# Performance work log

Hardware: AMD Instinct MI355X
Metric: run time of the kernel (lower is better)

The kernel has to match this reference:

```python
import jax, jax.numpy as jnp
import numpy as np

N_NODES = 50000
BN_EPS = 1e-5


def setup_inputs() -> dict:
    key = jax.random.key(0)
    ks = jax.random.split(key, 10)
    n, e, d, L = N_NODES, 500000, 128, 2
    x = jax.random.normal(ks[0], (n, d), dtype=jnp.float32)
    edge_index = jax.random.randint(ks[1], (2, e), 0, n, dtype=jnp.int64)
    edge_attr = jax.random.normal(ks[2], (e, d), dtype=jnp.float32)
    W1 = jax.random.normal(ks[3], (L, d, d), dtype=jnp.float32) * 0.05
    b1 = jax.random.normal(ks[4], (L, d), dtype=jnp.float32) * 0.02
    gamma = 1.0 + 0.1 * jax.random.normal(ks[5], (L, d), dtype=jnp.float32)
    beta = 0.1 * jax.random.normal(ks[6], (L, d), dtype=jnp.float32)
    W2 = jax.random.normal(ks[7], (L, d, d), dtype=jnp.float32) * 0.05
    b2 = jax.random.normal(ks[8], (L, d), dtype=jnp.float32) * 0.02
    return {"x": x, "edge_index": edge_index, "edge_attr": edge_attr,
            "W1": W1, "b1": b1, "gamma": gamma, "beta": beta, "W2": W2, "b2": b2}


def _gine_layer(x, src, dst, edge_attr, W1l, b1l, gl, bl, W2l, b2l):
    # GINEConv message: relu(x_j + edge_attr), sum-aggregated to target nodes
    msg = jax.nn.relu(x[src] + edge_attr)              # [E, d]
    agg = jax.ops.segment_sum(msg, dst, num_segments=N_NODES)  # [N, d]
    h = (x + agg) @ W1l + b1l                           # eps=0 -> (1+eps)*x = x
    # BatchNorm1d over nodes (train-mode batch stats, biased var)
    mu = jnp.mean(h, axis=0)
    var = jnp.mean(jnp.square(h - mu), axis=0)
    h = (h - mu) * jax.lax.rsqrt(var + BN_EPS) * gl + bl
    h = jax.nn.relu(h)
    h = jax.nn.relu(h @ W2l + b2l)
    return jax.nn.relu(h)  # encoder's outer activation


def reference(x, edge_index, edge_attr, W1, b1, gamma, beta, W2, b2):
    src, dst = edge_index[0], edge_index[1]
    L = W1.shape[0]
    for l in range(L):
        x = _gine_layer(x, src, dst, edge_attr, W1[l], b1[l], gamma[l], beta[l], W2[l], b2[l])
    return x
```

## Files before the change

kernel.cpp:

```cpp
#include <hip/hip_runtime.h>

#define BN_EPS 1e-5f

using f4 = __attribute__((ext_vector_type(4))) float;

__device__ inline f4 relu4(f4 v) {
    v.x = fmaxf(v.x, 0.f); v.y = fmaxf(v.y, 0.f);
    v.z = fmaxf(v.z, 0.f); v.w = fmaxf(v.w, 0.f);
    return v;
}

__global__ __launch_bounds__(256) void detect_i64_kernel(const int* __restrict__ ei,
                                                         int* __restrict__ flag, int npairs) {
    __shared__ int ok;
    if (threadIdx.x == 0) ok = 1;
    __syncthreads();
    bool bad = false;
    for (int i = threadIdx.x; i < npairs; i += 256)
        bad |= (ei[2 * i + 1] != 0);
    if (bad) ok = 0;
    __syncthreads();
    if (threadIdx.x == 0) *flag = ok;
}

__global__ __launch_bounds__(256) void canon_kernel(const int* __restrict__ ei,
                                                    const int* __restrict__ flag,
                                                    int* __restrict__ canon,
                                                    int* __restrict__ deg, int n2, int N) {
    int i = blockIdx.x * 256 + threadIdx.x;
    if (i < N) deg[i] = 0;
    if (i >= n2) return;
    int wide = *flag;
    canon[i] = wide ? ei[2 * i] : ei[i];
}

__global__ __launch_bounds__(256) void hist_kernel(const int* __restrict__ dst,
                                                   int* __restrict__ deg, int E) {
    int e = blockIdx.x * 256 + threadIdx.x;
    if (e >= E) return;
    atomicAdd(&deg[dst[e]], 1);
}

__global__ __launch_bounds__(1024) void scan_kernel(const int* __restrict__ deg,
                                                    int* __restrict__ rowptr,
                                                    int* __restrict__ cursor, int N) {
    __shared__ int part[1024];
    int t = threadIdx.x;
    int chunk = (N + 1023) / 1024;
    int lo = t * chunk;
    int hi = lo + chunk;
    if (lo > N) lo = N;
    if (hi > N) hi = N;
    int s = 0;
    for (int i = lo; i < hi; ++i) s += deg[i];
    part[t] = s;
    __syncthreads();
    for (int off = 1; off < 1024; off <<= 1) {
        int v = (t >= off) ? part[t - off] : 0;
        __syncthreads();
        part[t] += v;
        __syncthreads();
    }
    int run = (t == 0) ? 0 : part[t - 1];
    for (int i = lo; i < hi; ++i) { rowptr[i] = run; cursor[i] = run; run += deg[i]; }
    if (t == 1023) rowptr[N] = run;
}

__global__ __launch_bounds__(256) void fill_kernel(const int* __restrict__ src,
                                                   const int* __restrict__ dst,
                                                   int* __restrict__ cursor,
                                                   int2* __restrict__ pbuf, int E) {
    int e = blockIdx.x * 256 + threadIdx.x;
    if (e >= E) return;
    int d = dst[e];
    int pos = atomicAdd(&cursor[d], 1);
    pbuf[pos] = make_int2(e, src[e]);
}

__global__ __launch_bounds__(256) void gather_kernel(const float* __restrict__ x,
                                                     const float* __restrict__ ea,
                                                     const int* __restrict__ rowptr,
                                                     const int2* __restrict__ pbuf,
                                                     float* __restrict__ aggx,
                                                     float* __restrict__ sums, int N) {
    if (blockIdx.x == 0) sums[threadIdx.x] = 0.f;
    int t = blockIdx.x * 256 + threadIdx.x;
    int n = t >> 5;
    if (n >= N) return;
    int f = t & 31;
    int lo = rowptr[n], hi = rowptr[n + 1];
    f4 acc0 = ((const f4*)(x + (size_t)n * 128))[f];
    f4 acc1 = {0.f, 0.f, 0.f, 0.f};
    int i = lo;
    for (; i + 2 <= hi; i += 2) {
        int2 p0 = pbuf[i];
        int2 p1 = pbuf[i + 1];
        f4 xv0 = ((const f4*)(x + (size_t)p0.y * 128))[f];
        f4 av0 = __builtin_nontemporal_load(((const f4*)(ea + (size_t)p0.x * 128)) + f);
        f4 xv1 = ((const f4*)(x + (size_t)p1.y * 128))[f];
        f4 av1 = __builtin_nontemporal_load(((const f4*)(ea + (size_t)p1.x * 128)) + f);
        acc0 += relu4(xv0 + av0);
        acc1 += relu4(xv1 + av1);
    }
    if (i < hi) {
        int2 p0 = pbuf[i];
        f4 xv0 = ((const f4*)(x + (size_t)p0.y * 128))[f];
        f4 av0 = __builtin_nontemporal_load(((const f4*)(ea + (size_t)p0.x * 128)) + f);
        acc0 += relu4(xv0 + av0);
    }
    f4 r = acc0 + acc1;
    ((f4*)(aggx + (size_t)n * 128))[f] = r;
}

template <int MODE>
__global__ __launch_bounds__(256) void gemm_kernel(const float* __restrict__ A,
                                                   const float* __restrict__ W,
                                                   const float* __restrict__ bias,
                                                   float* __restrict__ sums,
                                                   const float* __restrict__ gamma,
                                                   const float* __restrict__ beta,
                                                   float* __restrict__ out, int N,
                                                   float invN) {
    __shared__ float sA[64][132];
    __shared__ float sW[32][128];
    __shared__ float sScale[128];
    __shared__ float sShift[128];
    int t = threadIdx.x;
    int rbase = blockIdx.x * 64;

    if (MODE == 2) {
        if (t < 128) {
            float mean = sums[t] * invN;
            float var = sums[128 + t] * invN - mean * mean;
            float inv = rsqrtf(var + BN_EPS);
            float sc = gamma[t] * inv;
            sScale[t] = sc;
            sShift[t] = beta[t] - mean * sc;
        }
        __syncthreads();
    }

    {
        int colq = t & 31;
        int r0 = t >> 5;
        float4 s4 = make_float4(0.f, 0.f, 0.f, 0.f), sh4 = make_float4(0.f, 0.f, 0.f, 0.f);
        if (MODE == 2) {
            s4 = reinterpret_cast<const float4*>(sScale)[colq];
            sh4 = reinterpret_cast<const float4*>(sShift)[colq];
        }
#pragma unroll
        for (int it = 0; it < 8; ++it) {
            int r = r0 + it * 8;
            int row = rbase + r;
            float4 v = make_float4(0.f, 0.f, 0.f, 0.f);
            if (row < N) {
                float4 a = reinterpret_cast<const float4*>(A + (size_t)row * 128)[colq];
                if (MODE == 1) {
                    v = a;
                } else {
                    v.x = fmaxf(a.x * s4.x + sh4.x, 0.f);
                    v.y = fmaxf(a.y * s4.y + sh4.y, 0.f);
                    v.z = fmaxf(a.z * s4.z + sh4.z, 0.f);
                    v.w = fmaxf(a.w * s4.w + sh4.w, 0.f);
                }
            }
            *reinterpret_cast<float4*>(&sA[r][colq * 4]) = v;
        }
    }

    float acc[4][8];
#pragma unroll
    for (int r = 0; r < 4; ++r)
#pragma unroll
        for (int c = 0; c < 8; ++c) acc[r][c] = 0.f;

    int cg = t & 15, rg = t >> 4;
    int c0a = cg * 4;
    int c0b = 64 + cg * 4;

    for (int kc = 0; kc < 4; ++kc) {
        __syncthreads();
#pragma unroll
        for (int pass = 0; pass < 4; ++pass) {
            int kk = (t >> 5) + pass * 8;
            int k = kc * 32 + kk;
            float4 w = reinterpret_cast<const float4*>(W + (size_t)k * 128)[t & 31];
            *reinterpret_cast<float4*>(&sW[kk][(t & 31) * 4]) = w;
        }
        __syncthreads();
#pragma unroll
        for (int kk0 = 0; kk0 < 32; kk0 += 4) {
            float4 a[4];
#pragma unroll
            for (int r = 0; r < 4; ++r)
                a[r] = *reinterpret_cast<const float4*>(&sA[rg * 4 + r][kc * 32 + kk0]);
#pragma unroll
            for (int j = 0; j < 4; ++j) {
                float4 w0 = *reinterpret_cast<const float4*>(&sW[kk0 + j][c0a]);
                float4 w1 = *reinterpret_cast<const float4*>(&sW[kk0 + j][c0b]);
#pragma unroll
                for (int r = 0; r < 4; ++r) {
                    float av = (j == 0) ? a[r].x : (j == 1) ? a[r].y : (j == 2) ? a[r].z : a[r].w;
                    acc[r][0] += av * w0.x;
                    acc[r][1] += av * w0.y;
                    acc[r][2] += av * w0.z;
                    acc[r][3] += av * w0.w;
                    acc[r][4] += av * w1.x;
                    acc[r][5] += av * w1.y;
                    acc[r][6] += av * w1.z;
                    acc[r][7] += av * w1.w;
                }
            }
        }
    }

    float4 b0 = *reinterpret_cast<const float4*>(bias + c0a);
    float4 b1v = *reinterpret_cast<const float4*>(bias + c0b);
    float cs[8], cs2[8];
#pragma unroll
    for (int j = 0; j < 8; ++j) { cs[j] = 0.f; cs2[j] = 0.f; }

#pragma unroll
    for (int r = 0; r < 4; ++r) {
        int row = rbase + rg * 4 + r;
        if (row >= N) continue;
        float4 o0, o1;
        o0.x = acc[r][0] + b0.x;  o0.y = acc[r][1] + b0.y;
        o0.z = acc[r][2] + b0.z;  o0.w = acc[r][3] + b0.w;
        o1.x = acc[r][4] + b1v.x; o1.y = acc[r][5] + b1v.y;
        o1.z = acc[r][6] + b1v.z; o1.w = acc[r][7] + b1v.w;
        if (MODE == 2) {
            o0.x = fmaxf(o0.x, 0.f); o0.y = fmaxf(o0.y, 0.f);
            o0.z = fmaxf(o0.z, 0.f); o0.w = fmaxf(o0.w, 0.f);
            o1.x = fmaxf(o1.x, 0.f); o1.y = fmaxf(o1.y, 0.f);
            o1.z = fmaxf(o1.z, 0.f); o1.w = fmaxf(o1.w, 0.f);
        } else {
            cs[0] += o0.x; cs2[0] += o0.x * o0.x;
            cs[1] += o0.y; cs2[1] += o0.y * o0.y;
            cs[2] += o0.z; cs2[2] += o0.z * o0.z;
            cs[3] += o0.w; cs2[3] += o0.w * o0.w;
            cs[4] += o1.x; cs2[4] += o1.x * o1.x;
            cs[5] += o1.y; cs2[5] += o1.y * o1.y;
            cs[6] += o1.z; cs2[6] += o1.z * o1.z;
            cs[7] += o1.w; cs2[7] += o1.w * o1.w;
        }
        *reinterpret_cast<float4*>(out + (size_t)row * 128 + c0a) = o0;
        *reinterpret_cast<float4*>(out + (size_t)row * 128 + c0b) = o1;
    }

    if (MODE == 1) {
        __syncthreads();
        float* red = &sA[0][0];
        float* red2 = red + 2048;
        int base = (rg * 16 + cg) * 8;
#pragma unroll
        for (int j = 0; j < 8; ++j) { red[base + j] = cs[j]; red2[base + j] = cs2[j]; }
        __syncthreads();
        if (t < 128) {
            int cgj = (t & 63) >> 2;
            int j = (t & 3) + ((t >> 6) << 2);
            float s = 0.f, s2 = 0.f;
#pragma unroll
            for (int rr = 0; rr < 16; ++rr) {
                s += red[(rr * 16 + cgj) * 8 + j];
                s2 += red2[(rr * 16 + cgj) * 8 + j];
            }
            unsafeAtomicAdd(&sums[t], s);
            unsafeAtomicAdd(&sums[128 + t], s2);
        }
    }
}

extern "C" void kernel_launch(void* const* d_in, const int* in_sizes, int n_in,
                              void* d_out, int out_size, void* d_ws, size_t ws_size,
                              hipStream_t stream) {
    const float* x     = (const float*)d_in[0];
    const int*   ei    = (const int*)d_in[1];
    const float* ea    = (const float*)d_in[2];
    const float* W1    = (const float*)d_in[3];
    const float* b1    = (const float*)d_in[4];
    const float* gamma = (const float*)d_in[5];
    const float* beta  = (const float*)d_in[6];
    const float* W2    = (const float*)d_in[7];
    const float* b2    = (const float*)d_in[8];

    int N = in_sizes[0] / 128;
    int E = in_sizes[2] / 128;
    int L = in_sizes[3] / (128 * 128);

    size_t NF = (size_t)N * 128;
    float* aggx  = (float*)d_ws;
    float* h     = aggx + NF;
    float* sums  = h + NF;
    int*   canon  = (int*)(sums + 256);
    int*   deg    = canon + (size_t)2 * E;
    int*   rowptr = deg + N;
    int*   cursor = rowptr + N + 2;
    int2*  pbuf   = (int2*)(cursor + N);
    int*   flag   = (int*)(pbuf + E);

    int npairs = (E < 4096) ? E : 4096;
    detect_i64_kernel<<<1, 256, 0, stream>>>(ei, flag, npairs);
    int E2 = 2 * E;
    int m = (E2 > N) ? E2 : N;
    canon_kernel<<<(m + 255) / 256, 256, 0, stream>>>(ei, flag, canon, deg, E2, N);
    const int* src = canon;
    const int* dst = canon + E;

    int eBlocks = (E + 255) / 256;
    hist_kernel<<<eBlocks, 256, 0, stream>>>(dst, deg, E);
    scan_kernel<<<1, 1024, 0, stream>>>(deg, rowptr, cursor, N);
    fill_kernel<<<eBlocks, 256, 0, stream>>>(src, dst, cursor, pbuf, E);

    int gatherBlocks = (N * 32 + 255) / 256;
    int gemmBlocks = (N + 63) / 64;
    float invN = 1.0f / (float)N;
    const float* xin = x;
    for (int l = 0; l < L; ++l) {
        float* xout = (float*)d_out;
        gather_kernel<<<gatherBlocks, 256, 0, stream>>>(xin, ea, rowptr, pbuf, aggx, sums, N);
        gemm_kernel<1><<<gemmBlocks, 256, 0, stream>>>(aggx, W1 + (size_t)l * 16384,
                                                       b1 + (size_t)l * 128, sums,
                                                       nullptr, nullptr, h, N, invN);
        gemm_kernel<2><<<gemmBlocks, 256, 0, stream>>>(h, W2 + (size_t)l * 16384,
                                                       b2 + (size_t)l * 128, sums,
                                                       gamma + (size_t)l * 128,
                                                       beta + (size_t)l * 128, xout, N, invN);
        xin = xout;
    }
}
```

Before: 777.7 us.

## Fuse degree histogram into canon, parallelize CSR scan, unroll gather by four

Moves zeroing of the degree array into the detect kernel and folds the destination histogram atomics into the canonicalization kernel, which removes one launch and one pass over dst. The single-block 1024-thread serial-chunk scan is replaced by a three-kernel multi-block scan (block scan, partials scan, add-back). The gather loop is unrolled to four edges with four accumulators to increase memory-level parallelism. This adds two small launches, and the single-block detect kernel now zeroes all N degrees serially over 256 threads.

```diff
diff --git a/kernel.cpp b/kernel.cpp
--- a/kernel.cpp
+++ b/kernel.cpp
@@ -11,7 +11,8 @@
 }
 
 __global__ __launch_bounds__(256) void detect_i64_kernel(const int* __restrict__ ei,
-                                                         int* __restrict__ flag, int npairs) {
+                                                         int* __restrict__ flag, int npairs,
+                                                         int* __restrict__ deg, int N) {
     __shared__ int ok;
     if (threadIdx.x == 0) ok = 1;
     __syncthreads();
@@ -19,6 +20,10 @@
     for (int i = threadIdx.x; i < npairs; i += 256)
         bad |= (ei[2 * i + 1] != 0);
     if (bad) ok = 0;
+    int nq = N >> 2;
+    int4* d4 = (int4*)deg;
+    for (int i = threadIdx.x; i < nq; i += 256) d4[i] = make_int4(0, 0, 0, 0);
+    for (int i = (nq << 2) + threadIdx.x; i < N; i += 256) deg[i] = 0;
     __syncthreads();
     if (threadIdx.x == 0) *flag = ok;
 }
@@ -26,44 +31,83 @@
 __global__ __launch_bounds__(256) void canon_kernel(const int* __restrict__ ei,
                                                     const int* __restrict__ flag,
                                                     int* __restrict__ canon,
-                                                    int* __restrict__ deg, int n2, int N) {
+                                                    int* __restrict__ deg, int n2, int E) {
     int i = blockIdx.x * 256 + threadIdx.x;
-    if (i < N) deg[i] = 0;
     if (i >= n2) return;
     int wide = *flag;
-    canon[i] = wide ? ei[2 * i] : ei[i];
-}
-
-__global__ __launch_bounds__(256) void hist_kernel(const int* __restrict__ dst,
-                                                   int* __restrict__ deg, int E) {
-    int e = blockIdx.x * 256 + threadIdx.x;
-    if (e >= E) return;
-    atomicAdd(&deg[dst[e]], 1);
-}
-
-__global__ __launch_bounds__(1024) void scan_kernel(const int* __restrict__ deg,
-                                                    int* __restrict__ rowptr,
-                                                    int* __restrict__ cursor, int N) {
-    __shared__ int part[1024];
+    int v = wide ? ei[2 * i] : ei[i];
+    canon[i] = v;
+    if (i >= E) atomicAdd(&deg[v], 1);
+}
+
+__global__ __launch_bounds__(256) void scan_blk_kernel(const int* __restrict__ deg,
+                                                       int* __restrict__ rowptr,
+                                                       int* __restrict__ partials, int N) {
+    __shared__ int s[256];
+    int b = blockIdx.x, t = threadIdx.x;
+    int base = b * 1024 + t * 4;
+    int4 v = make_int4(0, 0, 0, 0);
+    if (base + 3 < N) v = *(const int4*)(deg + base);
+    else {
+        if (base < N) v.x = deg[base];
+        if (base + 1 < N) v.y = deg[base + 1];
+        if (base + 2 < N) v.z = deg[base + 2];
+        if (base + 3 < N) v.w = deg[base + 3];
+    }
+    s[t] = v.x + v.y + v.z + v.w;
+    __syncthreads();
+    for (int off = 1; off < 256; off <<= 1) {
+        int u = (t >= off) ? s[t - off] : 0;
+        __syncthreads();
+        s[t] += u;
+        __syncthreads();
+    }
+    int excl = (t == 0) ? 0 : s[t - 1];
+    int4 w;
+    w.x = excl;
+    w.y = excl + v.x;
+    w.z = w.y + v.y;
+    w.w = w.z + v.z;
+    if (base + 3 < N) *(int4*)(rowptr + base) = w;
+    else {
+        if (base < N) rowptr[base] = w.x;
+        if (base + 1 < N) rowptr[base + 1] = w.y;
+        if (base + 2 < N) rowptr[base + 2] = w.z;
+        if (base + 3 < N) rowptr[base + 3] = w.w;
+    }
+    if (t == 255) partials[b] = s[255];
+}
+
+__global__ __launch_bounds__(256) void scan_part_kernel(int* __restrict__ partials, int nb) {
+    __shared__ int s[256];
     int t = threadIdx.x;
-    int chunk = (N + 1023) / 1024;
-    int lo = t * chunk;
-    int hi = lo + chunk;
-    if (lo > N) lo = N;
-    if (hi > N) hi = N;
-    int s = 0;
-    for (int i = lo; i < hi; ++i) s += deg[i];
-    part[t] = s;
-    __syncthreads();
-    for (int off = 1; off < 1024; off <<= 1) {
-        int v = (t >= off) ? part[t - off] : 0;
-        __syncthreads();
-        part[t] += v;
-        __syncthreads();
-    }
-    int run = (t == 0) ? 0 : part[t - 1];
-    for (int i = lo; i < hi; ++i) { rowptr[i] = run; cursor[i] = run; run += deg[i]; }
-    if (t == 1023) rowptr[N] = run;
+    if (nb <= 256) {
+        s[t] = (t < nb) ? partials[t] : 0;
+        __syncthreads();
+        for (int off = 1; off < 256; off <<= 1) {
+            int u = (t >= off) ? s[t - off] : 0;
+            __syncthreads();
+            s[t] += u;
+            __syncthreads();
+        }
+        if (t < nb) partials[t] = (t == 0) ? 0 : s[t - 1];
+    } else if (t == 0) {
+        int run = 0;
+        for (int i = 0; i < nb; ++i) { int d = partials[i]; partials[i] = run; run += d; }
+    }
+}
+
+__global__ __launch_bounds__(256) void scan_add_kernel(int* __restrict__ rowptr,
+                                                       int* __restrict__ cursor,
+                                                       const int* __restrict__ partials,
+                                                       int N, int E) {
+    int i = blockIdx.x * 256 + threadIdx.x;
+    if (i < N) {
+        int v = rowptr[i] + partials[i >> 10];
+        rowptr[i] = v;
+        cursor[i] = v;
+    }
+    if (i == N) rowptr[N] = E;
 }
 
 __global__ __launch_bounds__(256) void fill_kernel(const int* __restrict__ src,
@@ -91,24 +135,44 @@
     int lo = rowptr[n], hi = rowptr[n + 1];
     f4 acc0 = ((const f4*)(x + (size_t)n * 128))[f];
     f4 acc1 = {0.f, 0.f, 0.f, 0.f};
+    f4 acc2 = {0.f, 0.f, 0.f, 0.f};
+    f4 acc3 = {0.f, 0.f, 0.f, 0.f};
     int i = lo;
+    for (; i + 4 <= hi; i += 4) {
+        int2 q0 = pbuf[i];
+        int2 q1 = pbuf[i + 1];
+        int2 q2 = pbuf[i + 2];
+        int2 q3 = pbuf[i + 3];
+        f4 xa = ((const f4*)(x + (size_t)q0.y * 128))[f];
+        f4 aa = __builtin_nontemporal_load(((const f4*)(ea + (size_t)q0.x * 128)) + f);
+        f4 xb = ((const f4*)(x + (size_t)q1.y * 128))[f];
+        f4 ab = __builtin_nontemporal_load(((const f4*)(ea + (size_t)q1.x * 128)) + f);
+        f4 xc = ((const f4*)(x + (size_t)q2.y * 128))[f];
+        f4 ac = __builtin_nontemporal_load(((const f4*)(ea + (size_t)q2.x * 128)) + f);
+        f4 xd = ((const f4*)(x + (size_t)q3.y * 128))[f];
+        f4 ad = __builtin_nontemporal_load(((const f4*)(ea + (size_t)q3.x * 128)) + f);
+        acc0 += relu4(xa + aa);
+        acc1 += relu4(xb + ab);
+        acc2 += relu4(xc + ac);
+        acc3 += relu4(xd + ad);
+    }
     for (; i + 2 <= hi; i += 2) {
-        int2 p0 = pbuf[i];
-        int2 p1 = pbuf[i + 1];
-        f4 xv0 = ((const f4*)(x + (size_t)p0.y * 128))[f];
-        f4 av0 = __builtin_nontemporal_load(((const f4*)(ea + (size_t)p0.x * 128)) + f);
-        f4 xv1 = ((const f4*)(x + (size_t)p1.y * 128))[f];
-        f4 av1 = __builtin_nontemporal_load(((const f4*)(ea + (size_t)p1.x * 128)) + f);
-        acc0 += relu4(xv0 + av0);
-        acc1 += relu4(xv1 + av1);
+        int2 q0 = pbuf[i];
+        int2 q1 = pbuf[i + 1];
+        f4 xa = ((const f4*)(x + (size_t)q0.y * 128))[f];
+        f4 aa = __builtin_nontemporal_load(((const f4*)(ea + (size_t)q0.x * 128)) + f);
+        f4 xb = ((const f4*)(x + (size_t)q1.y * 128))[f];
+        f4 ab = __builtin_nontemporal_load(((const f4*)(ea + (size_t)q1.x * 128)) + f);
+        acc0 += relu4(xa + aa);
+        acc1 += relu4(xb + ab);
     }
     if (i < hi) {
-        int2 p0 = pbuf[i];
-        f4 xv0 = ((const f4*)(x + (size_t)p0.y * 128))[f];
-        f4 av0 = __builtin_nontemporal_load(((const f4*)(ea + (size_t)p0.x * 128)) + f);
-        acc0 += relu4(xv0 + av0);
-    }
-    f4 r = acc0 + acc1;
+        int2 q0 = pbuf[i];
+        f4 xa = ((const f4*)(x + (size_t)q0.y * 128))[f];
+        f4 aa = __builtin_nontemporal_load(((const f4*)(ea + (size_t)q0.x * 128)) + f);
+        acc0 += relu4(xa + aa);
+    }
+    f4 r = (acc0 + acc1) + (acc2 + acc3);
     ((f4*)(aggx + (size_t)n * 128))[f] = r;
 }
 
@@ -297,19 +361,21 @@
     int*   rowptr = deg + N;
     int*   cursor = rowptr + N + 2;
     int2*  pbuf   = (int2*)(cursor + N);
-    int*   flag   = (int*)(pbuf + E);
+    int*   partials = (int*)(pbuf + E);
+    int*   flag   = partials + ((N + 1023) / 1024) + 1;
 
     int npairs = (E < 4096) ? E : 4096;
-    detect_i64_kernel<<<1, 256, 0, stream>>>(ei, flag, npairs);
+    detect_i64_kernel<<<1, 256, 0, stream>>>(ei, flag, npairs, deg, N);
     int E2 = 2 * E;
-    int m = (E2 > N) ? E2 : N;
-    canon_kernel<<<(m + 255) / 256, 256, 0, stream>>>(ei, flag, canon, deg, E2, N);
+    canon_kernel<<<(E2 + 255) / 256, 256, 0, stream>>>(ei, flag, canon, deg, E2, E);
     const int* src = canon;
     const int* dst = canon + E;
 
+    int nb = (N + 1023) / 1024;
+    scan_blk_kernel<<<nb, 256, 0, stream>>>(deg, rowptr, partials, N);
+    scan_part_kernel<<<1, 256, 0, stream>>>(partials, nb);
+    scan_add_kernel<<<(N + 256) / 256, 256, 0, stream>>>(rowptr, cursor, partials, N, E);
     int eBlocks = (E + 255) / 256;
-    hist_kernel<<<eBlocks, 256, 0, stream>>>(dst, deg, E);
-    scan_kernel<<<1, 1024, 0, stream>>>(deg, rowptr, cursor, N);
     fill_kernel<<<eBlocks, 256, 0, stream>>>(src, dst, cursor, pbuf, E);
 
     int gatherBlocks = (N * 32 + 255) / 256;
```

Measured after the change: 677.3 us. 1.15x faster.
